# Kernel optimization log

Hardware: AMD Instinct MI355X
Metric: run time of the kernel (lower is better)

## Reference

```python
import jax, jax.numpy as jnp
import numpy as np

B, T, D = 4, 1024, 1024
H = 16
DH = D // H            # head dim (attention_dim/num_heads)
FF = 4096
EPS = 1e-6             # allennlp LayerNorm eps
NEG = jnp.finfo(jnp.float32).min


def _layer_norm(x, g, b):
    # allennlp LayerNorm: (x - mean) / (unbiased_std + eps) * gamma + beta
    mean = jnp.mean(x, axis=-1, keepdims=True)
    var = jnp.var(x, axis=-1, keepdims=True) * (x.shape[-1] / (x.shape[-1] - 1))
    return g * (x - mean) / (jnp.sqrt(var) + EPS) + b


def setup_inputs() -> dict:
    key = jax.random.key(0)
    ks = jax.random.split(key, 12)
    s = lambda fan_in: 1.0 / np.sqrt(fan_in)
    return {
        "src": jax.random.normal(ks[0], (B, T, D), jnp.float32),
        "src_mask": jnp.ones((B, T), jnp.int32),
        # weights stored [in, out]
        "q_w": jax.random.uniform(ks[1], (D, D), jnp.float32, -s(D), s(D)),
        "q_b": jnp.zeros((D,), jnp.float32),
        "kv_w": jax.random.uniform(ks[2], (D, 2 * D), jnp.float32, -s(D), s(D)),
        "kv_b": jnp.zeros((2 * D,), jnp.float32),
        "out_w": jax.random.uniform(ks[3], (D, D), jnp.float32, -s(D), s(D)),
        "out_b": jnp.zeros((D,), jnp.float32),
        "ffn_w1": jax.random.uniform(ks[4], (D, FF), jnp.float32, -s(D), s(D)),
        "ffn_b1": jnp.zeros((FF,), jnp.float32),
        "ffn_w2": jax.random.uniform(ks[5], (FF, D), jnp.float32, -s(FF), s(FF)),
        "ffn_b2": jnp.zeros((D,), jnp.float32),
        "norm1_g": jnp.ones((D,), jnp.float32),
        "norm1_b": jnp.zeros((D,), jnp.float32),
        "norm2_g": jnp.ones((D,), jnp.float32),
        "norm2_b": jnp.zeros((D,), jnp.float32),
    }


def reference(src, src_mask, q_w, q_b, kv_w, kv_b, out_w, out_b,
              ffn_w1, ffn_b1, ffn_w2, ffn_b2,
              norm1_g, norm1_b, norm2_g, norm2_b):
    b, t, d = src.shape
    scale = jnp.asarray(DH ** 0.5, src.dtype)

    q = (src @ q_w + q_b).reshape(b, t, H, DH)
    kv = src @ kv_w + kv_b                         # (b,t,2D): first half keys, second half values
    k = kv[..., :D].reshape(b, t, H, DH)
    v = kv[..., D:].reshape(b, t, H, DH)

    # scaled dot-product: queries divided by sqrt(head_dim) before bmm
    logits = jnp.einsum("bqhd,bkhd->bhqk", q / scale, k)
    # memory_efficient masked_softmax: masked key positions -> dtype min
    mask = src_mask[:, None, None, :].astype(bool)  # (b,1,1,t) over keys
    logits = jnp.where(mask, logits, NEG)
    attn = jax.nn.softmax(logits, axis=-1)          # dropout off (eval)

    ctx = jnp.einsum("bhqk,bkhd->bqhd", attn, v).reshape(b, t, D)
    attn_out = ctx @ out_w + out_b

    out1 = _layer_norm(src + attn_out, norm1_g, norm1_b)
    ffn = jax.nn.relu(out1 @ ffn_w1 + ffn_b1) @ ffn_w2 + ffn_b2
    out2 = _layer_norm(out1 + ffn, norm2_g, norm2_b)
    return out2
```

## Files before the change

kernel.cpp:

```cpp
#include <hip/hip_runtime.h>

#define DEV __device__ __forceinline__

typedef unsigned short u16;
typedef __attribute__((ext_vector_type(4))) float f32x4;
typedef __attribute__((ext_vector_type(8))) short short8;

DEV u16 f2bf(float f) {
  union { float f; unsigned u; } c; c.f = f;
  unsigned u = c.u;
  unsigned r = (u + 0x7FFFu + ((u >> 16) & 1u)) >> 16;
  return (u16)r;
}
DEV float bf2f(u16 h) {
  union { unsigned u; float f; } c; c.u = ((unsigned)h) << 16;
  return c.f;
}

DEV void gload16(const void* g, void* l) {
  __builtin_amdgcn_global_load_lds(
      (__attribute__((address_space(1))) void*)(g),
      (__attribute__((address_space(3))) void*)(l), 16, 0, 0);
}

__global__ __launch_bounds__(256) void cast_f32_bf16_kernel(
    const float* __restrict__ in, u16* __restrict__ out, int n4) {
  int i = blockIdx.x * blockDim.x + threadIdx.x;
  if (i >= n4) return;
  float4 v = reinterpret_cast<const float4*>(in)[i];
  ushort4 o;
  o.x = f2bf(v.x); o.y = f2bf(v.y); o.z = f2bf(v.z); o.w = f2bf(v.w);
  reinterpret_cast<ushort4*>(out)[i] = o;
}

template <typename TIN>
__global__ __launch_bounds__(256) void transpose_to_bf16_kernel(
    const TIN* __restrict__ in, int ld_in, int col_off,
    u16* __restrict__ out, int ld_out) {
  __shared__ float tile[32][33];
  int c0 = blockIdx.x * 32, r0 = blockIdx.y * 32;
  int tx = threadIdx.x, ty = threadIdx.y;
#pragma unroll
  for (int j = 0; j < 4; ++j) {
    int r = r0 + ty + j * 8;
    TIN raw = in[(size_t)r * ld_in + col_off + c0 + tx];
    float v;
    if constexpr (sizeof(TIN) == 4) v = (float)raw;
    else v = bf2f((u16)raw);
    tile[ty + j * 8][tx] = v;
  }
  __syncthreads();
#pragma unroll
  for (int j = 0; j < 4; ++j) {
    out[(size_t)(c0 + ty + j * 8) * ld_out + r0 + tx] = f2bf(tile[tx][ty + j * 8]);
  }
}

template <typename OutT, bool RELU>
__global__ __launch_bounds__(256) void gemm_bt_kernel(
    const u16* __restrict__ A, int lda,
    const u16* __restrict__ Bt, int ldb,
    const float* __restrict__ bias, const float* __restrict__ bias2, int split,
    OutT* __restrict__ C, int ldc, size_t c_off,
    int K, float scale) {
  __shared__ __align__(16) u16 lds[2][2][128 * 32];
  const int lane = threadIdx.x & 63;
  const int wid = threadIdx.x >> 6;
  const int wr = wid >> 1, wc = wid & 1;
  const int lr = lane & 15, hi = lane >> 4;
  const int rb = blockIdx.y, cb = blockIdx.x;
  const int z = blockIdx.z;
  const int r_in = lane >> 2;
  const int c_in = lane & 3;

  const u16* Abase = A + (size_t)(rb * 128) * lda + (size_t)z * K;
  const u16* Bbase = Bt + (size_t)(cb * 128) * ldb + (size_t)z * K;
  if (z != 0) bias = nullptr;
  C += (size_t)z * c_off;

  f32x4 acc[4][4];
  const f32x4 zero = {0.f, 0.f, 0.f, 0.f};
#pragma unroll
  for (int m = 0; m < 4; ++m)
#pragma unroll
    for (int n = 0; n < 4; ++n) acc[m][n] = zero;

  auto stage = [&](int bf, int t) {
#pragma unroll
    for (int j = 0; j < 2; ++j) {
      int r = wid * 16 + j * 64 + r_in;
      int csrc = c_in ^ ((r >> 1) & 3);
      gload16(Abase + (size_t)r * lda + t * 32 + csrc * 8,
              &lds[bf][0][(wid * 16 + j * 64) * 32]);
      gload16(Bbase + (size_t)r * ldb + t * 32 + csrc * 8,
              &lds[bf][1][(wid * 16 + j * 64) * 32]);
    }
  };

  const int sw = (lr >> 1) & 3;
  auto compute = [&](int bf) {
    const u16* la = lds[bf][0];
    const u16* lb = lds[bf][1];
    short8 af[4], bfr[4];
#pragma unroll
    for (int m = 0; m < 4; ++m)
      af[m] = *(const short8*)(la + (wr * 64 + m * 16 + lr) * 32 + ((hi ^ sw) * 8));
#pragma unroll
    for (int n = 0; n < 4; ++n)
      bfr[n] = *(const short8*)(lb + (wc * 64 + n * 16 + lr) * 32 + ((hi ^ sw) * 8));
#pragma unroll
    for (int m = 0; m < 4; ++m)
#pragma unroll
      for (int n = 0; n < 4; ++n)
        acc[m][n] = __builtin_amdgcn_mfma_f32_16x16x32_bf16(af[m], bfr[n], acc[m][n], 0, 0, 0);
  };

  const int NT = K >> 5;
  stage(0, 0);
  __syncthreads();
  int cur = 0;
  for (int t = 0; t < NT; ++t) {
    if (t + 1 < NT) stage(cur ^ 1, t + 1);
    compute(cur);
    __syncthreads();
    cur ^= 1;
  }

#pragma unroll
  for (int m = 0; m < 4; ++m) {
    int row0 = rb * 128 + wr * 64 + m * 16 + hi * 4;
#pragma unroll
    for (int n = 0; n < 4; ++n) {
      int col = cb * 128 + wc * 64 + n * 16 + lr;
      float bv = 0.0f, sc = scale;
      if (bias) {
        if (col < split) bv = bias[col];
        else { bv = bias2[col - split]; sc = 1.0f; }
      }
#pragma unroll
      for (int r = 0; r < 4; ++r) {
        float v = (acc[m][n][r] + bv) * sc;
        if (RELU) v = fmaxf(v, 0.0f);
        if constexpr (sizeof(OutT) == 2)
          C[(size_t)(row0 + r) * ldc + col] = f2bf(v);
        else
          C[(size_t)(row0 + r) * ldc + col] = v;
      }
    }
  }
}

__global__ __launch_bounds__(256) void attn_kernel(
    const u16* __restrict__ QKV, const u16* __restrict__ Vt,
    const int* __restrict__ mask, u16* __restrict__ CTX) {
  __shared__ __align__(16) u16 kl[2][64 * 64];
  __shared__ __align__(16) u16 vl[2][64 * 64];
  __shared__ __align__(16) u16 pl[4][32 * 64];
  const int lane = threadIdx.x & 63;
  const int wid = threadIdx.x >> 6;
  const int lr = lane & 15, hi = lane >> 4;
  const int bh = blockIdx.x, qt = blockIdx.y;
  const int b = bh >> 4, h = bh & 15;

  short8 qf[2][2];
#pragma unroll
  for (int m = 0; m < 2; ++m)
#pragma unroll
    for (int ks = 0; ks < 2; ++ks) {
      size_t grow = (size_t)(b * 1024 + qt * 128 + wid * 32 + m * 16 + lr);
      qf[m][ks] = *(const short8*)(QKV + grow * 3072 + h * 64 + ks * 32 + hi * 8);
    }

  unsigned long long keepm = 0ull;
#pragma unroll
  for (int kt = 0; kt < 16; ++kt)
#pragma unroll
    for (int n = 0; n < 4; ++n)
      if (mask[b * 1024 + kt * 64 + n * 16 + lr] != 0)
        keepm |= (1ull << (kt * 4 + n));

  const u16* Kbase = QKV + (size_t)(b * 1024) * 3072 + 1024 + h * 64;
  const u16* Vbase = Vt + (size_t)(h * 64) * 4096 + b * 1024;
  const int sr = lane >> 3;
  const int sc = lane & 7;

  auto stage = [&](int bf, int kt) {
#pragma unroll
    for (int j = 0; j < 2; ++j) {
      int r = wid * 16 + j * 8 + sr;
      int cs = sc ^ (r & 7);
      gload16(Kbase + (size_t)(kt * 64 + r) * 3072 + cs * 8,
              &kl[bf][(wid * 16 + j * 8) * 64]);
      gload16(Vbase + (size_t)r * 4096 + kt * 64 + cs * 8,
              &vl[bf][(wid * 16 + j * 8) * 64]);
    }
  };

  float m_run[2][4], l_run[2][4];
  f32x4 O[2][4];
  const f32x4 zero = {0.f, 0.f, 0.f, 0.f};
#pragma unroll
  for (int m = 0; m < 2; ++m) {
#pragma unroll
    for (int r = 0; r < 4; ++r) { m_run[m][r] = -3.0e38f; l_run[m][r] = 0.f; }
#pragma unroll
    for (int d = 0; d < 4; ++d) O[m][d] = zero;
  }

  stage(0, 0);
  __syncthreads();
  int cur = 0;
  for (int kt = 0; kt < 16; ++kt) {
    if (kt + 1 < 16) stage(cur ^ 1, kt + 1);

    short8 kf[4][2];
#pragma unroll
    for (int n = 0; n < 4; ++n) {
      int key = n * 16 + lr;
#pragma unroll
      for (int ks = 0; ks < 2; ++ks) {
        int ch = (hi + 4 * ks) ^ (key & 7);
        kf[n][ks] = *(const short8*)(kl[cur] + key * 64 + ch * 8);
      }
    }
    f32x4 s[2][4];
#pragma unroll
    for (int m = 0; m < 2; ++m)
#pragma unroll
      for (int n = 0; n < 4; ++n) s[m][n] = zero;
#pragma unroll
    for (int ks = 0; ks < 2; ++ks)
#pragma unroll
      for (int m = 0; m < 2; ++m)
#pragma unroll
        for (int n = 0; n < 4; ++n)
          s[m][n] = __builtin_amdgcn_mfma_f32_16x16x32_bf16(qf[m][ks], kf[n][ks], s[m][n], 0, 0, 0);

    bool keep[4];
#pragma unroll
    for (int n = 0; n < 4; ++n)
      keep[n] = (keepm >> (kt * 4 + n)) & 1ull;

#pragma unroll
    for (int m = 0; m < 2; ++m) {
#pragma unroll
      for (int r = 0; r < 4; ++r) {
        float sv[4];
#pragma unroll
        for (int n = 0; n < 4; ++n) {
          float x = s[m][n][r];
          sv[n] = keep[n] ? x : -3.0e38f;
        }
        float tm = fmaxf(fmaxf(sv[0], sv[1]), fmaxf(sv[2], sv[3]));
        tm = fmaxf(tm, __shfl_xor(tm, 1));
        tm = fmaxf(tm, __shfl_xor(tm, 2));
        tm = fmaxf(tm, __shfl_xor(tm, 4));
        tm = fmaxf(tm, __shfl_xor(tm, 8));
        float mo = m_run[m][r];
        float mn = fmaxf(mo, tm);
        float alpha = __expf(mo - mn);
        m_run[m][r] = mn;
        int prow = m * 16 + hi * 4 + r;
        float ps = 0.f;
        u16 pb[4];
#pragma unroll
        for (int n = 0; n < 4; ++n) {
          float p = __expf(sv[n] - mn);
          ps += p;
          pb[n] = f2bf(p);
        }
        l_run[m][r] = l_run[m][r] * alpha + ps;
#pragma unroll
        for (int d = 0; d < 4; ++d) O[m][d][r] *= alpha;
#pragma unroll
        for (int n = 0; n < 4; ++n) {
          int col = n * 16 + lr;
          int ch = (col >> 3) ^ (prow & 7);
          pl[wid][prow * 64 + ch * 8 + (col & 7)] = pb[n];
        }
      }
    }

#pragma unroll
    for (int ks = 0; ks < 2; ++ks) {
      short8 pa[2], vf[4];
#pragma unroll
      for (int m = 0; m < 2; ++m) {
        int prow = m * 16 + lr;
        int ch = (hi + 4 * ks) ^ (prow & 7);
        pa[m] = *(const short8*)(pl[wid] + prow * 64 + ch * 8);
      }
#pragma unroll
      for (int d = 0; d < 4; ++d) {
        int vrow = d * 16 + lr;
        int ch = (hi + 4 * ks) ^ (vrow & 7);
        vf[d] = *(const short8*)(vl[cur] + vrow * 64 + ch * 8);
      }
#pragma unroll
      for (int m = 0; m < 2; ++m)
#pragma unroll
        for (int d = 0; d < 4; ++d)
          O[m][d] = __builtin_amdgcn_mfma_f32_16x16x32_bf16(pa[m], vf[d], O[m][d], 0, 0, 0);
    }
    __syncthreads();
    cur ^= 1;
  }

#pragma unroll
  for (int m = 0; m < 2; ++m) {
#pragma unroll
    for (int r = 0; r < 4; ++r) {
      float l = l_run[m][r];
      l += __shfl_xor(l, 1);
      l += __shfl_xor(l, 2);
      l += __shfl_xor(l, 4);
      l += __shfl_xor(l, 8);
      float inv = 1.0f / l;
      size_t row = (size_t)(b * 1024 + qt * 128 + wid * 32 + m * 16 + hi * 4 + r);
#pragma unroll
      for (int d = 0; d < 4; ++d)
        CTX[row * 1024 + h * 64 + d * 16 + lr] = f2bf(O[m][d][r] * inv);
    }
  }
}

__global__ __launch_bounds__(256) void ln_kernel(
    const float* __restrict__ xa, const float* __restrict__ xb,
    const float* __restrict__ xc,
    const float* __restrict__ g, const float* __restrict__ beta,
    float* __restrict__ of, u16* __restrict__ ob) {
  int row = blockIdx.x;
  int tid = threadIdx.x;
  const float* pa = xa + (size_t)row * 1024;
  const float* pb = xb + (size_t)row * 1024;
  const float* pc = xc ? xc + (size_t)row * 1024 : nullptr;
  float v[4];
  float s = 0.f, s2 = 0.f;
#pragma unroll
  for (int j = 0; j < 4; ++j) {
    int c = tid + j * 256;
    float x = pa[c] + pb[c];
    if (pc) x += pc[c];
    v[j] = x; s += x; s2 += x * x;
  }
#pragma unroll
  for (int d = 1; d < 64; d <<= 1) {
    s += __shfl_xor(s, d);
    s2 += __shfl_xor(s2, d);
  }
  __shared__ float red[8];
  int w = tid >> 6, lane = tid & 63;
  if (lane == 0) { red[w] = s; red[4 + w] = s2; }
  __syncthreads();
  s = red[0] + red[1] + red[2] + red[3];
  s2 = red[4] + red[5] + red[6] + red[7];
  float mean = s * (1.0f / 1024.0f);
  float var = fmaxf((s2 - 1024.0f * mean * mean) * (1.0f / 1023.0f), 0.0f);
  float rden = 1.0f / (sqrtf(var) + 1e-6f);
#pragma unroll
  for (int j = 0; j < 4; ++j) {
    int c = tid + j * 256;
    float y = g[c] * (v[j] - mean) * rden + beta[c];
    of[(size_t)row * 1024 + c] = y;
    if (ob) ob[(size_t)row * 1024 + c] = f2bf(y);
  }
}

extern "C" void kernel_launch(void* const* d_in, const int* in_sizes, int n_in,
                              void* d_out, int out_size, void* d_ws, size_t ws_size,
                              hipStream_t stream) {
  const float* src   = (const float*)d_in[0];
  const int*   mask  = (const int*)d_in[1];
  const float* q_w   = (const float*)d_in[2];
  const float* q_b   = (const float*)d_in[3];
  const float* kv_w  = (const float*)d_in[4];
  const float* kv_b  = (const float*)d_in[5];
  const float* out_w = (const float*)d_in[6];
  const float* out_b = (const float*)d_in[7];
  const float* w1    = (const float*)d_in[8];
  const float* b1    = (const float*)d_in[9];
  const float* w2    = (const float*)d_in[10];
  const float* b2    = (const float*)d_in[11];
  const float* g1    = (const float*)d_in[12];
  const float* be1   = (const float*)d_in[13];
  const float* g2    = (const float*)d_in[14];
  const float* be2   = (const float*)d_in[15];
  float* out = (float*)d_out;

  char* ws = (char*)d_ws;
  const size_t MB = 1024 * 1024;
  const int BIG = 1 << 30;
  u16*  Xbf   = (u16*)(ws + 0);
  u16*  CTX   = (u16*)(ws + 8 * MB);
  u16*  WqkvT = (u16*)(ws + 16 * MB);
  u16*  WoT   = (u16*)(ws + 22 * MB);
  u16*  W1T   = (u16*)(ws + 24 * MB);
  u16*  W2T   = (u16*)(ws + 32 * MB);
  u16*  QKV   = (u16*)(ws + 40 * MB);
  u16*  Vt    = (u16*)(ws + 64 * MB);
  u16*  F1b   = (u16*)(ws + 40 * MB);
  float* AOUT = (float*)(ws + 72 * MB);
  float* OUT1F= (float*)(ws + 88 * MB);
  u16*  OUT1B = (u16*)(ws + 104 * MB);
  float* P0   = (float*)(ws + 0);
  float* P1   = (float*)(ws + 72 * MB);

  cast_f32_bf16_kernel<<<dim3(4096), dim3(256), 0, stream>>>(src, Xbf, 1024 * 1024);
  transpose_to_bf16_kernel<float><<<dim3(32, 32), dim3(32, 8), 0, stream>>>(q_w, 1024, 0, WqkvT, 1024);
  transpose_to_bf16_kernel<float><<<dim3(64, 32), dim3(32, 8), 0, stream>>>(kv_w, 2048, 0, WqkvT + (size_t)1024 * 1024, 1024);
  transpose_to_bf16_kernel<float><<<dim3(32, 32), dim3(32, 8), 0, stream>>>(out_w, 1024, 0, WoT, 1024);
  transpose_to_bf16_kernel<float><<<dim3(128, 32), dim3(32, 8), 0, stream>>>(w1, 4096, 0, W1T, 1024);
  transpose_to_bf16_kernel<float><<<dim3(32, 128), dim3(32, 8), 0, stream>>>(w2, 1024, 0, W2T, 4096);
  gemm_bt_kernel<u16, false><<<dim3(24, 32), dim3(256), 0, stream>>>(
      Xbf, 1024, WqkvT, 1024, q_b, kv_b, 1024, QKV, 3072, 0, 1024, 0.125f);
  transpose_to_bf16_kernel<u16><<<dim3(32, 128), dim3(32, 8), 0, stream>>>(QKV, 3072, 2048, Vt, 4096);
  attn_kernel<<<dim3(64, 8), dim3(256), 0, stream>>>(QKV, Vt, mask, CTX);
  gemm_bt_kernel<float, false><<<dim3(8, 32), dim3(256), 0, stream>>>(
      CTX, 1024, WoT, 1024, out_b, nullptr, BIG, AOUT, 1024, 0, 1024, 1.0f);
  ln_kernel<<<dim3(4096), dim3(256), 0, stream>>>(src, AOUT, nullptr, g1, be1, OUT1F, OUT1B);
  gemm_bt_kernel<u16, true><<<dim3(32, 32), dim3(256), 0, stream>>>(
      OUT1B, 1024, W1T, 1024, b1, nullptr, BIG, F1b, 4096, 0, 1024, 1.0f);
  gemm_bt_kernel<float, false><<<dim3(8, 32, 2), dim3(256), 0, stream>>>(
      F1b, 4096, W2T, 4096, b2, nullptr, BIG, P0, 1024,
      (size_t)(P1 - P0), 2048, 1.0f);
  ln_kernel<<<dim3(4096), dim3(256), 0, stream>>>(OUT1F, P0, P1, g2, be2, out, nullptr);
  (void)in_sizes; (void)n_in; (void)out_size; (void)ws_size;
}
```

Measured before the change: 378.9 us.

## Rework GEMMs with 4-slot LDS ring pipeline, XCD remap, and fused prep kernel

Replaces the double-buffered GEMM with a templated 4-slot LDS ring that keeps three k-tiles in flight, using explicit vmcnt waits, sched barriers and setprio around the MFMAs. Workgroup IDs are remapped across XCDs for locality, and the QKV and FFN1 GEMMs use larger 256x256 tiles. The five weight transposes and the input cast are fused into one prep kernel to cut launch overhead. The FFN2 split-K is dropped in favour of a single full-K pass. The risks are higher LDS and register pressure and less parallelism for FFN2.

After: 347.2 us. 8.4% less time.

```diff
diff --git a/kernel.cpp b/kernel.cpp
--- a/kernel.cpp
+++ b/kernel.cpp
@@ -1,6 +1,7 @@
 #include <hip/hip_runtime.h>
 
 #define DEV __device__ __forceinline__
+#define SB0 __builtin_amdgcn_sched_barrier(0)
 
 typedef unsigned short u16;
 typedef __attribute__((ext_vector_type(4))) float f32x4;
@@ -22,20 +23,44 @@
       (__attribute__((address_space(1))) void*)(g),
       (__attribute__((address_space(3))) void*)(l), 16, 0, 0);
 }
-
-__global__ __launch_bounds__(256) void cast_f32_bf16_kernel(
-    const float* __restrict__ in, u16* __restrict__ out, int n4) {
-  int i = blockIdx.x * blockDim.x + threadIdx.x;
-  if (i >= n4) return;
-  float4 v = reinterpret_cast<const float4*>(in)[i];
-  ushort4 o;
-  o.x = f2bf(v.x); o.y = f2bf(v.y); o.z = f2bf(v.z); o.w = f2bf(v.w);
-  reinterpret_cast<ushort4*>(out)[i] = o;
-}
-
-template <typename TIN>
-__global__ __launch_bounds__(256) void transpose_to_bf16_kernel(
-    const TIN* __restrict__ in, int ld_in, int col_off,
+DEV void vmc8() { asm volatile("s_waitcnt vmcnt(8)" ::: "memory"); SB0; }
+DEV void vmc0() { asm volatile("s_waitcnt vmcnt(0)" ::: "memory"); SB0; }
+
+__global__ __launch_bounds__(256) void prep_kernel(
+    const float* __restrict__ src, const float* __restrict__ q_w,
+    const float* __restrict__ kv_w, const float* __restrict__ out_w,
+    const float* __restrict__ w1, const float* __restrict__ w2,
+    u16* __restrict__ Xbf, u16* __restrict__ WqkvT, u16* __restrict__ WoT,
+    u16* __restrict__ W1T, u16* __restrict__ W2T) {
+  __shared__ float tile[32 * 33];
+  int bb = blockIdx.x, tid = threadIdx.x;
+  if (bb < 4096) {
+    int i = bb * 256 + tid;
+    float4 v = reinterpret_cast<const float4*>(src)[i];
+    ushort4 o;
+    o.x = f2bf(v.x); o.y = f2bf(v.y); o.z = f2bf(v.z); o.w = f2bf(v.w);
+    reinterpret_cast<ushort4*>(Xbf)[i] = o;
+    return;
+  }
+  const float* in; u16* outp; int ld_in, ld_out, bx, by;
+  if (bb < 5120)       { int t = bb - 4096;  in = q_w;   outp = WqkvT; ld_in = 1024; ld_out = 1024; bx = t & 31;  by = t >> 5; }
+  else if (bb < 7168)  { int t = bb - 5120;  in = kv_w;  outp = WqkvT + (size_t)1024 * 1024; ld_in = 2048; ld_out = 1024; bx = t & 63;  by = t >> 6; }
+  else if (bb < 8192)  { int t = bb - 7168;  in = out_w; outp = WoT;   ld_in = 1024; ld_out = 1024; bx = t & 31;  by = t >> 5; }
+  else if (bb < 12288) { int t = bb - 8192;  in = w1;    outp = W1T;   ld_in = 4096; ld_out = 1024; bx = t & 127; by = t >> 7; }
+  else                 { int t = bb - 12288; in = w2;    outp = W2T;   ld_in = 1024; ld_out = 4096; bx = t & 31;  by = t >> 5; }
+  int tx = tid & 31, ty = tid >> 5;
+  int c0 = bx * 32, r0 = by * 32;
+#pragma unroll
+  for (int j = 0; j < 4; ++j)
+    tile[(ty + j * 8) * 33 + tx] = in[(size_t)(r0 + ty + j * 8) * ld_in + c0 + tx];
+  __syncthreads();
+#pragma unroll
+  for (int j = 0; j < 4; ++j)
+    outp[(size_t)(c0 + ty + j * 8) * ld_out + r0 + tx] = f2bf(tile[tx * 33 + ty + j * 8]);
+}
+
+__global__ __launch_bounds__(256) void transpose_u16_kernel(
+    const u16* __restrict__ in, int ld_in, int col_off,
     u16* __restrict__ out, int ld_out) {
   __shared__ float tile[32][33];
   int c0 = blockIdx.x * 32, r0 = blockIdx.y * 32;
@@ -43,100 +68,97 @@
 #pragma unroll
   for (int j = 0; j < 4; ++j) {
     int r = r0 + ty + j * 8;
-    TIN raw = in[(size_t)r * ld_in + col_off + c0 + tx];
-    float v;
-    if constexpr (sizeof(TIN) == 4) v = (float)raw;
-    else v = bf2f((u16)raw);
-    tile[ty + j * 8][tx] = v;
+    tile[ty + j * 8][tx] = bf2f(in[(size_t)r * ld_in + col_off + c0 + tx]);
   }
   __syncthreads();
 #pragma unroll
-  for (int j = 0; j < 4; ++j) {
+  for (int j = 0; j < 4; ++j)
     out[(size_t)(c0 + ty + j * 8) * ld_out + r0 + tx] = f2bf(tile[tx][ty + j * 8]);
-  }
-}
-
-template <typename OutT, bool RELU>
-__global__ __launch_bounds__(256) void gemm_bt_kernel(
+}
+
+template <int BM, int NWARP, typename OutT, bool RELU>
+__global__ __launch_bounds__(NWARP * 64, 2) void gemm_ring_kernel(
     const u16* __restrict__ A, int lda,
     const u16* __restrict__ Bt, int ldb,
     const float* __restrict__ bias, const float* __restrict__ bias2, int split,
-    OutT* __restrict__ C, int ldc, size_t c_off,
-    int K, float scale) {
-  __shared__ __align__(16) u16 lds[2][2][128 * 32];
-  const int lane = threadIdx.x & 63;
-  const int wid = threadIdx.x >> 6;
-  const int wr = wid >> 1, wc = wid & 1;
+    OutT* __restrict__ C, int ldc, int K, float scale) {
+  constexpr int MT = BM / 32;
+  constexpr int PWR = BM / 2;
+  constexpr int WN = NWARP / 2;
+  constexpr int SLOT = 2 * BM * 32;
+  __shared__ __align__(16) u16 ring[4][SLOT];
+
+  const int tid = threadIdx.x;
+  const int lane = tid & 63, wid = tid >> 6;
+  const int wr = wid / WN, wc = wid % WN;
   const int lr = lane & 15, hi = lane >> 4;
-  const int rb = blockIdx.y, cb = blockIdx.x;
-  const int z = blockIdx.z;
-  const int r_in = lane >> 2;
-  const int c_in = lane & 3;
-
-  const u16* Abase = A + (size_t)(rb * 128) * lda + (size_t)z * K;
-  const u16* Bbase = Bt + (size_t)(cb * 128) * ldb + (size_t)z * K;
-  if (z != 0) bias = nullptr;
-  C += (size_t)z * c_off;
-
-  f32x4 acc[4][4];
+
+  const int gx = gridDim.x;
+  const int nwg = gx * gridDim.y;
+  const int orig = blockIdx.y * gx + blockIdx.x;
+  const int q = nwg >> 3, r8 = nwg & 7, xcd = orig & 7, oo = orig >> 3;
+  const int lid = (xcd < r8 ? xcd * (q + 1) : r8 * (q + 1) + (xcd - r8) * q) + oo;
+  const int rb = lid / gx, cb = lid % gx;
+
+  const u16* Abase = A + (size_t)rb * BM * lda;
+  const u16* Bbase = Bt + (size_t)cb * BM * ldb;
+
+  auto stage = [&](int slot, int kt) {
+#pragma unroll
+    for (int j = 0; j < 2; ++j) {
+      int ch = wid * 2 + j;
+      int row = ch * 16 + (lane >> 2);
+      int cs = (lane & 3) ^ ((row >> 1) & 3);
+      gload16(Abase + (size_t)row * lda + kt * 32 + cs * 8, &ring[slot][ch * 512]);
+      gload16(Bbase + (size_t)row * ldb + kt * 32 + cs * 8, &ring[slot][BM * 32 + ch * 512]);
+    }
+  };
+
+  f32x4 acc[MT][4];
   const f32x4 zero = {0.f, 0.f, 0.f, 0.f};
 #pragma unroll
-  for (int m = 0; m < 4; ++m)
+  for (int m = 0; m < MT; ++m)
 #pragma unroll
     for (int n = 0; n < 4; ++n) acc[m][n] = zero;
 
-  auto stage = [&](int bf, int t) {
-#pragma unroll
-    for (int j = 0; j < 2; ++j) {
-      int r = wid * 16 + j * 64 + r_in;
-      int csrc = c_in ^ ((r >> 1) & 3);
-      gload16(Abase + (size_t)r * lda + t * 32 + csrc * 8,
-              &lds[bf][0][(wid * 16 + j * 64) * 32]);
-      gload16(Bbase + (size_t)r * ldb + t * 32 + csrc * 8,
-              &lds[bf][1][(wid * 16 + j * 64) * 32]);
-    }
-  };
+  const int NT = K >> 5;
+  stage(0, 0); stage(1, 1); stage(2, 2);
+  vmc8();
+  __builtin_amdgcn_s_barrier(); SB0;
 
   const int sw = (lr >> 1) & 3;
-  auto compute = [&](int bf) {
-    const u16* la = lds[bf][0];
-    const u16* lb = lds[bf][1];
-    short8 af[4], bfr[4];
-#pragma unroll
-    for (int m = 0; m < 4; ++m)
-      af[m] = *(const short8*)(la + (wr * 64 + m * 16 + lr) * 32 + ((hi ^ sw) * 8));
+  for (int k = 0; k < NT; ++k) {
+    const u16* la = &ring[k & 3][0];
+    const u16* lb = &ring[k & 3][BM * 32];
+    short8 bf[4], af[MT];
 #pragma unroll
     for (int n = 0; n < 4; ++n)
-      bfr[n] = *(const short8*)(lb + (wc * 64 + n * 16 + lr) * 32 + ((hi ^ sw) * 8));
-#pragma unroll
-    for (int m = 0; m < 4; ++m)
+      bf[n] = *(const short8*)(lb + (wc * 64 + n * 16 + lr) * 32 + ((hi ^ sw) * 8));
+#pragma unroll
+    for (int m = 0; m < MT; ++m)
+      af[m] = *(const short8*)(la + (wr * PWR + m * 16 + lr) * 32 + ((hi ^ sw) * 8));
+    if (k + 3 < NT) stage((k + 3) & 3, k + 3);
+    __builtin_amdgcn_s_setprio(1);
+#pragma unroll
+    for (int m = 0; m < MT; ++m)
 #pragma unroll
       for (int n = 0; n < 4; ++n)
-        acc[m][n] = __builtin_amdgcn_mfma_f32_16x16x32_bf16(af[m], bfr[n], acc[m][n], 0, 0, 0);
-  };
-
-  const int NT = K >> 5;
-  stage(0, 0);
-  __syncthreads();
-  int cur = 0;
-  for (int t = 0; t < NT; ++t) {
-    if (t + 1 < NT) stage(cur ^ 1, t + 1);
-    compute(cur);
-    __syncthreads();
-    cur ^= 1;
-  }
-
-#pragma unroll
-  for (int m = 0; m < 4; ++m) {
-    int row0 = rb * 128 + wr * 64 + m * 16 + hi * 4;
+        acc[m][n] = __builtin_amdgcn_mfma_f32_16x16x32_bf16(af[m], bf[n], acc[m][n], 0, 0, 0);
+    __builtin_amdgcn_s_setprio(0);
+    if (k + 4 < NT) vmc8();
+    else if (k + 1 < NT) vmc0();
+    __builtin_amdgcn_s_barrier(); SB0;
+  }
+
+#pragma unroll
+  for (int m = 0; m < MT; ++m) {
+    int row0 = rb * BM + wr * PWR + m * 16 + hi * 4;
 #pragma unroll
     for (int n = 0; n < 4; ++n) {
-      int col = cb * 128 + wc * 64 + n * 16 + lr;
+      int col = cb * BM + wc * 64 + n * 16 + lr;
       float bv = 0.0f, sc = scale;
-      if (bias) {
-        if (col < split) bv = bias[col];
-        else { bv = bias2[col - split]; sc = 1.0f; }
-      }
+      if (col < split) bv = bias[col];
+      else { bv = bias2[col - split]; sc = 1.0f; }
 #pragma unroll
       for (int r = 0; r < 4; ++r) {
         float v = (acc[m][n][r] + bv) * sc;
@@ -402,27 +424,21 @@
   float* AOUT = (float*)(ws + 72 * MB);
   float* OUT1F= (float*)(ws + 88 * MB);
   u16*  OUT1B = (u16*)(ws + 104 * MB);
-  float* P0   = (float*)(ws + 0);
-  float* P1   = (float*)(ws + 72 * MB);
-
-  cast_f32_bf16_kernel<<<dim3(4096), dim3(256), 0, stream>>>(src, Xbf, 1024 * 1024);
-  transpose_to_bf16_kernel<float><<<dim3(32, 32), dim3(32, 8), 0, stream>>>(q_w, 1024, 0, WqkvT, 1024);
-  transpose_to_bf16_kernel<float><<<dim3(64, 32), dim3(32, 8), 0, stream>>>(kv_w, 2048, 0, WqkvT + (size_t)1024 * 1024, 1024);
-  transpose_to_bf16_kernel<float><<<dim3(32, 32), dim3(32, 8), 0, stream>>>(out_w, 1024, 0, WoT, 1024);
-  transpose_to_bf16_kernel<float><<<dim3(128, 32), dim3(32, 8), 0, stream>>>(w1, 4096, 0, W1T, 1024);
-  transpose_to_bf16_kernel<float><<<dim3(32, 128), dim3(32, 8), 0, stream>>>(w2, 1024, 0, W2T, 4096);
-  gemm_bt_kernel<u16, false><<<dim3(24, 32), dim3(256), 0, stream>>>(
-      Xbf, 1024, WqkvT, 1024, q_b, kv_b, 1024, QKV, 3072, 0, 1024, 0.125f);
-  transpose_to_bf16_kernel<u16><<<dim3(32, 128), dim3(32, 8), 0, stream>>>(QKV, 3072, 2048, Vt, 4096);
+  float* F2F  = (float*)(ws + 72 * MB);
+
+  prep_kernel<<<dim3(16384), dim3(256), 0, stream>>>(
+      src, q_w, kv_w, out_w, w1, w2, Xbf, WqkvT, WoT, W1T, W2T);
+  gemm_ring_kernel<256, 8, u16, false><<<dim3(12, 16), dim3(512), 0, stream>>>(
+      Xbf, 1024, WqkvT, 1024, q_b, kv_b, 1024, QKV, 3072, 1024, 0.125f);
+  transpose_u16_kernel<<<dim3(32, 128), dim3(32, 8), 0, stream>>>(QKV, 3072, 2048, Vt, 4096);
   attn_kernel<<<dim3(64, 8), dim3(256), 0, stream>>>(QKV, Vt, mask, CTX);
-  gemm_bt_kernel<float, false><<<dim3(8, 32), dim3(256), 0, stream>>>(
-      CTX, 1024, WoT, 1024, out_b, nullptr, BIG, AOUT, 1024, 0, 1024, 1.0f);
+  gemm_ring_kernel<128, 4, float, false><<<dim3(8, 32), dim3(256), 0, stream>>>(
+      CTX, 1024, WoT, 1024, out_b, nullptr, BIG, AOUT, 1024, 1024, 1.0f);
   ln_kernel<<<dim3(4096), dim3(256), 0, stream>>>(src, AOUT, nullptr, g1, be1, OUT1F, OUT1B);
-  gemm_bt_kernel<u16, true><<<dim3(32, 32), dim3(256), 0, stream>>>(
-      OUT1B, 1024, W1T, 1024, b1, nullptr, BIG, F1b, 4096, 0, 1024, 1.0f);
-  gemm_bt_kernel<float, false><<<dim3(8, 32, 2), dim3(256), 0, stream>>>(
-      F1b, 4096, W2T, 4096, b2, nullptr, BIG, P0, 1024,
-      (size_t)(P1 - P0), 2048, 1.0f);
-  ln_kernel<<<dim3(4096), dim3(256), 0, stream>>>(OUT1F, P0, P1, g2, be2, out, nullptr);
+  gemm_ring_kernel<256, 8, u16, true><<<dim3(16, 16), dim3(512), 0, stream>>>(
+      OUT1B, 1024, W1T, 1024, b1, nullptr, BIG, F1b, 4096, 1024, 1.0f);
+  gemm_ring_kernel<128, 4, float, false><<<dim3(8, 32), dim3(256), 0, stream>>>(
+      F1b, 4096, W2T, 4096, b2, nullptr, BIG, F2F, 1024, 4096, 1.0f);
+  ln_kernel<<<dim3(4096), dim3(256), 0, stream>>>(OUT1F, F2F, nullptr, g2, be2, out, nullptr);
   (void)in_sizes; (void)n_in; (void)out_size; (void)ws_size;
 }
```
